# Kernel optimization log

Measured on AMD Instinct MI355X. Metric: run time of the kernel, lower is better.

## Reference

```python
import jax, jax.numpy as jnp
import numpy as np

HEAD_DIM = 64

def setup_inputs() -> dict:
    key = jax.random.key(0)
    k1, k2, k3, k4 = jax.random.split(key, 4)
    B, S, D, H = 8, 2048, 1024, HEAD_DIM
    x = jax.random.normal(k1, (B, S, D), dtype=jnp.float32)
    scale = 1.0 / np.sqrt(D)
    W_q = jax.random.normal(k2, (H, D), dtype=jnp.float32) * scale
    W_k = jax.random.normal(k3, (H, D), dtype=jnp.float32) * scale
    W_v = jax.random.normal(k4, (H, D), dtype=jnp.float32) * scale
    return {"input_embeddings": x, "W_q": W_q, "W_k": W_k, "W_v": W_v}

def reference(input_embeddings, W_q, W_k, W_v):
    # Linear(model_dim, head_dim, bias=False): y = x @ W.T
    q = jnp.einsum('bsd,hd->bsh', input_embeddings, W_q)
    k = jnp.einsum('bsd,hd->bsh', input_embeddings, W_k)
    v = jnp.einsum('bsd,hd->bsh', input_embeddings, W_v)
    scores = jnp.einsum('bqh,bkh->bqk', q, k) / jnp.sqrt(jnp.float32(HEAD_DIM))
    S = scores.shape[-1]
    causal = jnp.tril(jnp.ones((S, S), dtype=bool))  # [S,S]
    scores = jnp.where(causal, scores, -jnp.inf)
    attn = jax.nn.softmax(scores, axis=-1)
    # dropout p=0.0 (eval-equivalent): identity
    return jnp.einsum('bqk,bkh->bqh', attn, v)
```

## Files before the change

### kernel.cpp

```cpp
#include <hip/hip_runtime.h>
#include <hip/hip_bf16.h>

typedef __bf16 bf16x8 __attribute__((ext_vector_type(8)));
typedef __bf16 bf16x4 __attribute__((ext_vector_type(4)));
typedef float  f32x4  __attribute__((ext_vector_type(4)));

#define NB  8
#define SEQ 2048
#define DM  1024
#define HD  64

#define WAITV5 asm volatile("s_waitcnt vmcnt(5)" ::: "memory")
#define WAITV0 asm volatile("s_waitcnt vmcnt(0)" ::: "memory")

__device__ __forceinline__ void gll16(const void* g, void* l) {
    __builtin_amdgcn_global_load_lds(
        (const __attribute__((address_space(1))) unsigned int*)g,
        (__attribute__((address_space(3))) unsigned int*)l, 16, 0, 0);
}

__global__ void k_convw(const float* __restrict__ Wq, const float* __restrict__ Wk,
                        const float* __restrict__ Wv, __bf16* __restrict__ Wb) {
    int idx = blockIdx.x * blockDim.x + threadIdx.x;
    int e = idx * 4;
    const float* src;
    if (e < 65536)       src = Wq + e;
    else if (e < 131072) src = Wk + (e - 65536);
    else                 src = Wv + (e - 131072);
    float4 v = *reinterpret_cast<const float4*>(src);
    bf16x4 o;
    o[0] = (__bf16)v.x; o[1] = (__bf16)v.y; o[2] = (__bf16)v.z; o[3] = (__bf16)v.w;
    *reinterpret_cast<bf16x4*>(Wb + e) = o;
}

__launch_bounds__(512)
__global__ void k_proj(const float* __restrict__ X, const __bf16* __restrict__ Wb,
                       __bf16* __restrict__ Qb, __bf16* __restrict__ Kb,
                       __bf16* __restrict__ Vt) {
    __shared__ __align__(16) float  Xs[3][4096];
    __shared__ __align__(16) __bf16 Ws[3][12288];
    const int tid = threadIdx.x;
    const int w = tid >> 6, l = tid & 63;
    const int lr = l & 15, lg = l >> 4;
    const int wm = w >> 2, wn = w & 3;
    const int m0 = blockIdx.x * 64;

    const float* xsrc[2];
    #pragma unroll
    for (int j = 0; j < 2; ++j) {
        int ux = w * 128 + j * 64 + l;
        int r_ = ux >> 4, c_ = ux & 15;
        xsrc[j] = X + (size_t)(m0 + r_) * DM + (c_ ^ (r_ & 15)) * 4;
    }
    const __bf16* wsrc[3];
    #pragma unroll
    for (int j = 0; j < 3; ++j) {
        int uw = w * 192 + j * 64 + l;
        int r_ = uw >> 3, c_ = uw & 7;
        wsrc[j] = Wb + (size_t)r_ * DM + (c_ ^ (r_ & 7)) * 8;
    }

    f32x4 acc[2][3];
    #pragma unroll
    for (int mt = 0; mt < 2; ++mt)
        #pragma unroll
        for (int ct = 0; ct < 3; ++ct)
            acc[mt][ct] = f32x4{0.f, 0.f, 0.f, 0.f};

    int abase[2], bbase[3];
    #pragma unroll
    for (int mt = 0; mt < 2; ++mt) abase[mt] = (wm * 32 + mt * 16 + lr) * 64;
    #pragma unroll
    for (int ct = 0; ct < 3; ++ct) bbase[ct] = ((wn * 3 + ct) * 16 + lr) * 64;

    #pragma unroll
    for (int t = 0; t < 2; ++t) {
        #pragma unroll
        for (int j = 0; j < 2; ++j) gll16(xsrc[j] + t * 64, &Xs[t][w * 512 + j * 256]);
        #pragma unroll
        for (int j = 0; j < 3; ++j) gll16(wsrc[j] + t * 64, &Ws[t][w * 1536 + j * 512]);
    }

    int sl = 0;
    for (int t = 0; t < 16; ++t) {
        if (t < 15) WAITV5; else WAITV0;
        __builtin_amdgcn_s_barrier();
        if (t + 2 < 16) {
            int si = sl + 2; if (si >= 3) si -= 3;
            #pragma unroll
            for (int j = 0; j < 2; ++j)
                gll16(xsrc[j] + (t + 2) * 64, &Xs[si][w * 512 + j * 256]);
            #pragma unroll
            for (int j = 0; j < 3; ++j)
                gll16(wsrc[j] + (t + 2) * 64, &Ws[si][w * 1536 + j * 512]);
        }
        const float*  Xp = &Xs[sl][0];
        const __bf16* Wp = &Ws[sl][0];
        #pragma unroll
        for (int ks = 0; ks < 2; ++ks) {
            bf16x8 af[2];
            #pragma unroll
            for (int mt = 0; mt < 2; ++mt) {
                f32x4 a0 = *reinterpret_cast<const f32x4*>(Xp + abase[mt] + ((ks * 8 + lg * 2)     ^ lr) * 4);
                f32x4 a1 = *reinterpret_cast<const f32x4*>(Xp + abase[mt] + ((ks * 8 + lg * 2 + 1) ^ lr) * 4);
                #pragma unroll
                for (int j = 0; j < 4; ++j) { af[mt][j] = (__bf16)a0[j]; af[mt][4 + j] = (__bf16)a1[j]; }
            }
            #pragma unroll
            for (int ct = 0; ct < 3; ++ct) {
                bf16x8 bf = *reinterpret_cast<const bf16x8*>(
                    Wp + bbase[ct] + (((ks * 4 + lg) ^ (lr & 7)) * 8));
                #pragma unroll
                for (int mt = 0; mt < 2; ++mt)
                    acc[mt][ct] = __builtin_amdgcn_mfma_f32_16x16x32_bf16(af[mt], bf, acc[mt][ct], 0, 0, 0);
            }
        }
        ++sl; if (sl >= 3) sl = 0;
    }

    #pragma unroll
    for (int mt = 0; mt < 2; ++mt) {
        const int rowbase = m0 + wm * 32 + mt * 16 + lg * 4;
        #pragma unroll
        for (int ct = 0; ct < 3; ++ct) {
            const int ntile = wn * 3 + ct;
            const int mtx = ntile >> 2;
            const int d = (ntile & 3) * 16 + lr;
            if (mtx == 0) {
                #pragma unroll
                for (int r = 0; r < 4; ++r)
                    Qb[(size_t)(rowbase + r) * HD + d] = (__bf16)(acc[mt][ct][r] * 0.18033688f);
            } else if (mtx == 1) {
                #pragma unroll
                for (int r = 0; r < 4; ++r)
                    Kb[(size_t)(rowbase + r) * HD + d] = (__bf16)acc[mt][ct][r];
            } else {
                int bb = rowbase >> 11;
                int s0 = rowbase & 2047;
                bf16x4 vv;
                #pragma unroll
                for (int r = 0; r < 4; ++r) vv[r] = (__bf16)acc[mt][ct][r];
                *reinterpret_cast<bf16x4*>(Vt + ((size_t)bb * HD + d) * SEQ + s0) = vv;
            }
        }
    }
}

__launch_bounds__(512)
__global__ void k_attn(const __bf16* __restrict__ Qb, const __bf16* __restrict__ Kb,
                       const __bf16* __restrict__ Vt, __bf16* __restrict__ Opart,
                       float* __restrict__ ML, int T, int NC) {
    const int bid = blockIdx.x;
    const int b = bid / (16 * NC);
    const int rem = bid - b * 16 * NC;
    const int qt2 = rem / NC;
    const int c = rem - qt2 * NC;
    const int kmax = 2 * qt2 + 1;
    if (c * T > kmax) return;
    const int kt0 = c * T;
    const int nt = min(T, kmax + 1 - kt0);
    const int q0 = qt2 * 128;

    __shared__ __align__(16) __bf16 Ks[64][72];
    __shared__ __align__(16) __bf16 Vs[64][72];
    __shared__ __align__(16) __bf16 Ps[128][72];
    const int tid = threadIdx.x;
    const int w = tid >> 6, l = tid & 63;
    const int lr = l & 15, lg = l >> 4;
    const __bf16* Qp = Qb + (size_t)b * SEQ * HD;
    const __bf16* Kp = Kb + (size_t)b * SEQ * HD;
    const __bf16* Vp = Vt + (size_t)b * HD * SEQ;

    const int srow = tid >> 3, sc8 = (tid & 7) * 8;
    const int myq = q0 + 16 * w + lr;

    bf16x8 qa[2];
    #pragma unroll
    for (int ks = 0; ks < 2; ++ks)
        qa[ks] = *reinterpret_cast<const bf16x8*>(
            Qp + (size_t)myq * HD + ks * 32 + lg * 8);

    bf16x8 kpre, vpre;
    {
        const int k0 = kt0 * 64;
        kpre = *reinterpret_cast<const bf16x8*>(Kp + (size_t)(k0 + srow) * HD + sc8);
        vpre = *reinterpret_cast<const bf16x8*>(Vp + (size_t)srow * SEQ + k0 + sc8);
    }

    f32x4 oacc[4];
    #pragma unroll
    for (int r = 0; r < 4; ++r) oacc[r] = f32x4{0.f, 0.f, 0.f, 0.f};
    float m = -1e30f, lsum = 0.f;

    for (int it = 0; it < nt; ++it) {
        const int kt = kt0 + it;
        const int k0 = kt * 64;
        __syncthreads();
        *reinterpret_cast<bf16x8*>(&Ks[srow][sc8]) = kpre;
        *reinterpret_cast<bf16x8*>(&Vs[srow][sc8]) = vpre;
        __syncthreads();
        if (it + 1 < nt) {
            const int k0n = k0 + 64;
            kpre = *reinterpret_cast<const bf16x8*>(Kp + (size_t)(k0n + srow) * HD + sc8);
            vpre = *reinterpret_cast<const bf16x8*>(Vp + (size_t)srow * SEQ + k0n + sc8);
        }

        if (k0 > q0 + 16 * w + 15) continue;

        f32x4 sacc[4];
        #pragma unroll
        for (int t = 0; t < 4; ++t) sacc[t] = f32x4{0.f, 0.f, 0.f, 0.f};
        #pragma unroll
        for (int ks = 0; ks < 2; ++ks) {
            #pragma unroll
            for (int t = 0; t < 4; ++t) {
                bf16x8 kf = *reinterpret_cast<const bf16x8*>(&Ks[16 * t + lr][ks * 32 + lg * 8]);
                sacc[t] = __builtin_amdgcn_mfma_f32_16x16x32_bf16(kf, qa[ks], sacc[t], 0, 0, 0);
            }
        }

        float pmax = -1e30f;
        if (k0 + 63 > q0 + 16 * w) {
            #pragma unroll
            for (int t = 0; t < 4; ++t)
                #pragma unroll
                for (int r = 0; r < 4; ++r) {
                    float v = sacc[t][r];
                    if ((k0 + 16 * t + lg * 4 + r) > myq) v = -1e30f;
                    sacc[t][r] = v;
                    pmax = fmaxf(pmax, v);
                }
        } else {
            #pragma unroll
            for (int t = 0; t < 4; ++t)
                #pragma unroll
                for (int r = 0; r < 4; ++r) pmax = fmaxf(pmax, sacc[t][r]);
        }
        pmax = fmaxf(pmax, __shfl_xor(pmax, 16));
        pmax = fmaxf(pmax, __shfl_xor(pmax, 32));

        if (!__all(pmax <= m + 12.f)) {
            float mnew = fmaxf(m, pmax);
            float fsc = exp2f(m - mnew);
            m = mnew;
            lsum *= fsc;
            #pragma unroll
            for (int r = 0; r < 4; ++r) {
                float fq = __shfl(fsc, (l & 48) + lg * 4 + r);
                #pragma unroll
                for (int t2 = 0; t2 < 4; ++t2) oacc[t2][r] *= fq;
            }
        }

        float rs = 0.f;
        #pragma unroll
        for (int t = 0; t < 4; ++t)
            #pragma unroll
            for (int r = 0; r < 4; ++r) {
                float p = exp2f(sacc[t][r] - m);
                sacc[t][r] = p;
                rs += p;
            }
        rs += __shfl_xor(rs, 16);
        rs += __shfl_xor(rs, 32);
        lsum += rs;

        #pragma unroll
        for (int t = 0; t < 4; ++t) {
            bf16x4 pv;
            #pragma unroll
            for (int r = 0; r < 4; ++r) pv[r] = (__bf16)sacc[t][r];
            *reinterpret_cast<bf16x4*>(&Ps[16 * w + lr][16 * t + lg * 4]) = pv;
        }

        #pragma unroll
        for (int ks = 0; ks < 2; ++ks) {
            bf16x8 pa = *reinterpret_cast<const bf16x8*>(&Ps[16 * w + lr][ks * 32 + lg * 8]);
            #pragma unroll
            for (int t2 = 0; t2 < 4; ++t2) {
                bf16x8 vb = *reinterpret_cast<const bf16x8*>(&Vs[16 * t2 + lr][ks * 32 + lg * 8]);
                oacc[t2] = __builtin_amdgcn_mfma_f32_16x16x32_bf16(pa, vb, oacc[t2], 0, 0, 0);
            }
        }
    }

    const size_t slot = (size_t)bid;
    __bf16* op = Opart + slot * 8192;
    #pragma unroll
    for (int t2 = 0; t2 < 4; ++t2)
        #pragma unroll
        for (int r = 0; r < 4; ++r)
            op[(16 * w + lg * 4 + r) * 64 + 16 * t2 + lr] = (__bf16)oacc[t2][r];
    if (lg == 0) {
        float* ml = ML + slot * 256;
        int row = 16 * w + lr;
        ml[row * 2]     = m;
        ml[row * 2 + 1] = lsum;
    }
}

__launch_bounds__(512)
__global__ void k_merge(const __bf16* __restrict__ Opart, const float* __restrict__ ML,
                        float* __restrict__ Out, int T, int NC) {
    const int bq2 = blockIdx.x >> 1;
    const int half = blockIdx.x & 1;
    const int qt2 = bq2 & 15;
    const int nc = (2 * qt2 + 1) / T + 1;
    const int tid = threadIdx.x;
    const int row = tid >> 2;
    const int cg = (tid & 3) * 8 + half * 32;
    const int base = bq2 * NC;

    float M = -1e30f;
    for (int c = 0; c < nc; ++c)
        M = fmaxf(M, ML[(size_t)(base + c) * 256 + row * 2]);

    float L = 0.f;
    f32x4 a0{0,0,0,0}, a1{0,0,0,0};
    for (int c = 0; c < nc; ++c) {
        const float* ml = ML + (size_t)(base + c) * 256 + row * 2;
        float wgt = exp2f(ml[0] - M);
        L += ml[1] * wgt;
        bf16x8 v = *reinterpret_cast<const bf16x8*>(
            Opart + (size_t)(base + c) * 8192 + row * 64 + cg);
        #pragma unroll
        for (int j = 0; j < 4; ++j) {
            a0[j] += wgt * (float)v[j];
            a1[j] += wgt * (float)v[4 + j];
        }
    }
    float inv = 1.f / L;
    #pragma unroll
    for (int j = 0; j < 4; ++j) { a0[j] *= inv; a1[j] *= inv; }
    float* o = Out + ((size_t)bq2 * 128 + row) * 64 + cg;
    *reinterpret_cast<f32x4*>(o)     = a0;
    *reinterpret_cast<f32x4*>(o + 4) = a1;
}

extern "C" void kernel_launch(void* const* d_in, const int* in_sizes, int n_in,
                              void* d_out, int out_size, void* d_ws, size_t ws_size,
                              hipStream_t stream) {
    const float* x  = (const float*)d_in[0];
    const float* wq = (const float*)d_in[1];
    const float* wk = (const float*)d_in[2];
    const float* wv = (const float*)d_in[3];
    char* ws = (char*)d_ws;
    __bf16* Wb = (__bf16*)ws;
    __bf16* Qb = (__bf16*)(ws + 524288);
    __bf16* Kb = (__bf16*)(ws + 524288 + 2097152);
    __bf16* Vt = (__bf16*)(ws + 524288 + 2 * 2097152);
    const size_t base = 524288 + 3 * 2097152;
    float* out = (float*)d_out;

    int NC = (ws_size >= base + (size_t)(8 * 16 * 8) * 17408) ? 8 : 2;
    int T = 32 / NC;
    const int slots = 8 * 16 * NC;
    float*  ML    = (float*)(ws + base);
    __bf16* Opart = (__bf16*)(ws + base + (size_t)slots * 1024);

    hipLaunchKernelGGL(k_convw, dim3(192), dim3(256), 0, stream, wq, wk, wv, Wb);
    hipLaunchKernelGGL(k_proj,  dim3(256), dim3(512), 0, stream, x, Wb, Qb, Kb, Vt);
    hipLaunchKernelGGL(k_attn,  dim3(8 * 16 * NC), dim3(512), 0, stream,
                       Qb, Kb, Vt, Opart, ML, T, NC);
    hipLaunchKernelGGL(k_merge, dim3(256), dim3(512), 0, stream, Opart, ML, out, T, NC);
}
```

Before: 59.76 us.

## Restructure QKV projection: smaller row tiles, W fragments loaded straight to registers

The projection kernel now processes 32 rows per block with 4 waves, each wave owning all rows and 3 output column tiles. Weight fragments are read from global memory (L2-resident) directly into registers with double buffering, so only X goes through LDS via async loads. The grid doubles to 512 blocks. This cuts LDS footprint and traffic to raise occupancy and spread the X-read-bound projection across more CUs, at the cost of redundant per-wave W reads from L2 and more register pressure.

Result: slower. 67.11 us (+12.3%).

```diff
diff --git a/kernel.cpp b/kernel.cpp
--- a/kernel.cpp
+++ b/kernel.cpp
@@ -9,9 +9,6 @@
 #define SEQ 2048
 #define DM  1024
 #define HD  64
-
-#define WAITV5 asm volatile("s_waitcnt vmcnt(5)" ::: "memory")
-#define WAITV0 asm volatile("s_waitcnt vmcnt(0)" ::: "memory")
 
 __device__ __forceinline__ void gll16(const void* g, void* l) {
     __builtin_amdgcn_global_load_lds(
@@ -33,32 +30,62 @@
     *reinterpret_cast<bf16x4*>(Wb + e) = o;
 }
 
-__launch_bounds__(512)
+__device__ __forceinline__ void loadW(const __bf16* const (&wptr)[3], int t,
+                                      bf16x8 (&fr)[6]) {
+    #pragma unroll
+    for (int ct = 0; ct < 3; ++ct)
+        #pragma unroll
+        for (int ks = 0; ks < 2; ++ks)
+            fr[ct * 2 + ks] = *reinterpret_cast<const bf16x8*>(
+                wptr[ct] + (size_t)t * 64 + ks * 32);
+}
+
+__device__ __forceinline__ void computeT(const float* xb, int lr, int lg,
+                                         const bf16x8 (&fr)[6], f32x4 (&acc)[2][3]) {
+    #pragma unroll
+    for (int ks = 0; ks < 2; ++ks) {
+        bf16x8 af[2];
+        #pragma unroll
+        for (int mt = 0; mt < 2; ++mt) {
+            const int base = (mt * 16 + lr) * 64;
+            f32x4 a0 = *reinterpret_cast<const f32x4*>(xb + base + ((ks * 8 + lg * 2)     ^ lr) * 4);
+            f32x4 a1 = *reinterpret_cast<const f32x4*>(xb + base + ((ks * 8 + lg * 2 + 1) ^ lr) * 4);
+            #pragma unroll
+            for (int j = 0; j < 4; ++j) { af[mt][j] = (__bf16)a0[j]; af[mt][4 + j] = (__bf16)a1[j]; }
+        }
+        #pragma unroll
+        for (int ct = 0; ct < 3; ++ct)
+            #pragma unroll
+            for (int mt = 0; mt < 2; ++mt)
+                acc[mt][ct] = __builtin_amdgcn_mfma_f32_16x16x32_bf16(
+                    af[mt], fr[ct * 2 + ks], acc[mt][ct], 0, 0, 0);
+    }
+}
+
+__launch_bounds__(256)
 __global__ void k_proj(const float* __restrict__ X, const __bf16* __restrict__ Wb,
                        __bf16* __restrict__ Qb, __bf16* __restrict__ Kb,
                        __bf16* __restrict__ Vt) {
-    __shared__ __align__(16) float  Xs[3][4096];
-    __shared__ __align__(16) __bf16 Ws[3][12288];
+    __shared__ __align__(16) float Xs[3][2048];
     const int tid = threadIdx.x;
     const int w = tid >> 6, l = tid & 63;
     const int lr = l & 15, lg = l >> 4;
-    const int wm = w >> 2, wn = w & 3;
-    const int m0 = blockIdx.x * 64;
+    const int m0 = blockIdx.x * 32;
 
     const float* xsrc[2];
+    float* lb[2];
     #pragma unroll
     for (int j = 0; j < 2; ++j) {
-        int ux = w * 128 + j * 64 + l;
-        int r_ = ux >> 4, c_ = ux & 15;
+        int u = w * 64 + j * 256 + l;
+        int r_ = u >> 4, c_ = u & 15;
         xsrc[j] = X + (size_t)(m0 + r_) * DM + (c_ ^ (r_ & 15)) * 4;
-    }
-    const __bf16* wsrc[3];
-    #pragma unroll
-    for (int j = 0; j < 3; ++j) {
-        int uw = w * 192 + j * 64 + l;
-        int r_ = uw >> 3, c_ = uw & 7;
-        wsrc[j] = Wb + (size_t)r_ * DM + (c_ ^ (r_ & 7)) * 8;
-    }
+        lb[j]   = &Xs[0][0] + (w * 64 + j * 256) * 4;
+    }
+
+    const __bf16* wptr[3];
+    #pragma unroll
+    for (int ct = 0; ct < 3; ++ct)
+        wptr[ct] = Wb + (size_t)((w * 3 + ct) * 16 + lr) * DM + lg * 8;
 
     f32x4 acc[2][3];
     #pragma unroll
@@ -67,63 +94,50 @@
         for (int ct = 0; ct < 3; ++ct)
             acc[mt][ct] = f32x4{0.f, 0.f, 0.f, 0.f};
 
-    int abase[2], bbase[3];
-    #pragma unroll
-    for (int mt = 0; mt < 2; ++mt) abase[mt] = (wm * 32 + mt * 16 + lr) * 64;
-    #pragma unroll
-    for (int ct = 0; ct < 3; ++ct) bbase[ct] = ((wn * 3 + ct) * 16 + lr) * 64;
-
-    #pragma unroll
-    for (int t = 0; t < 2; ++t) {
-        #pragma unroll
-        for (int j = 0; j < 2; ++j) gll16(xsrc[j] + t * 64, &Xs[t][w * 512 + j * 256]);
-        #pragma unroll
-        for (int j = 0; j < 3; ++j) gll16(wsrc[j] + t * 64, &Ws[t][w * 1536 + j * 512]);
-    }
-
-    int sl = 0;
-    for (int t = 0; t < 16; ++t) {
-        if (t < 15) WAITV5; else WAITV0;
+    bf16x8 wA[6], wB[6];
+
+    #pragma unroll
+    for (int j = 0; j < 2; ++j) gll16(xsrc[j], lb[j]);
+    asm volatile("" ::: "memory");
+    loadW(wptr, 0, wA);
+    asm volatile("" ::: "memory");
+    #pragma unroll
+    for (int j = 0; j < 2; ++j) gll16(xsrc[j] + 64, lb[j] + 2048);
+
+    #pragma unroll
+    for (int tt = 0; tt < 7; ++tt) {
+        const int t0 = 2 * tt;
+        asm volatile("s_waitcnt vmcnt(8)" ::: "memory");
         __builtin_amdgcn_s_barrier();
-        if (t + 2 < 16) {
-            int si = sl + 2; if (si >= 3) si -= 3;
-            #pragma unroll
-            for (int j = 0; j < 2; ++j)
-                gll16(xsrc[j] + (t + 2) * 64, &Xs[si][w * 512 + j * 256]);
-            #pragma unroll
-            for (int j = 0; j < 3; ++j)
-                gll16(wsrc[j] + (t + 2) * 64, &Ws[si][w * 1536 + j * 512]);
-        }
-        const float*  Xp = &Xs[sl][0];
-        const __bf16* Wp = &Ws[sl][0];
-        #pragma unroll
-        for (int ks = 0; ks < 2; ++ks) {
-            bf16x8 af[2];
-            #pragma unroll
-            for (int mt = 0; mt < 2; ++mt) {
-                f32x4 a0 = *reinterpret_cast<const f32x4*>(Xp + abase[mt] + ((ks * 8 + lg * 2)     ^ lr) * 4);
-                f32x4 a1 = *reinterpret_cast<const f32x4*>(Xp + abase[mt] + ((ks * 8 + lg * 2 + 1) ^ lr) * 4);
-                #pragma unroll
-                for (int j = 0; j < 4; ++j) { af[mt][j] = (__bf16)a0[j]; af[mt][4 + j] = (__bf16)a1[j]; }
-            }
-            #pragma unroll
-            for (int ct = 0; ct < 3; ++ct) {
-                bf16x8 bf = *reinterpret_cast<const bf16x8*>(
-                    Wp + bbase[ct] + (((ks * 4 + lg) ^ (lr & 7)) * 8));
-                #pragma unroll
-                for (int mt = 0; mt < 2; ++mt)
-                    acc[mt][ct] = __builtin_amdgcn_mfma_f32_16x16x32_bf16(af[mt], bf, acc[mt][ct], 0, 0, 0);
-            }
-        }
-        ++sl; if (sl >= 3) sl = 0;
-    }
+        loadW(wptr, t0 + 1, wB);
+        asm volatile("" ::: "memory");
+        #pragma unroll
+        for (int j = 0; j < 2; ++j)
+            gll16(xsrc[j] + (size_t)(t0 + 2) * 64, lb[j] + ((t0 + 2) % 3) * 2048);
+        computeT(&Xs[t0 % 3][0], lr, lg, wA, acc);
+        asm volatile("s_waitcnt vmcnt(8)" ::: "memory");
+        __builtin_amdgcn_s_barrier();
+        loadW(wptr, t0 + 2, wA);
+        asm volatile("" ::: "memory");
+        #pragma unroll
+        for (int j = 0; j < 2; ++j)
+            gll16(xsrc[j] + (size_t)(t0 + 3) * 64, lb[j] + ((t0 + 3) % 3) * 2048);
+        computeT(&Xs[(t0 + 1) % 3][0], lr, lg, wB, acc);
+    }
+    asm volatile("s_waitcnt vmcnt(8)" ::: "memory");
+    __builtin_amdgcn_s_barrier();
+    loadW(wptr, 15, wB);
+    computeT(&Xs[14 % 3][0], lr, lg, wA, acc);
+    asm volatile("s_waitcnt vmcnt(0)" ::: "memory");
+    __builtin_amdgcn_s_barrier();
+    computeT(&Xs[15 % 3][0], lr, lg, wB, acc);
 
     #pragma unroll
     for (int mt = 0; mt < 2; ++mt) {
-        const int rowbase = m0 + wm * 32 + mt * 16 + lg * 4;
+        const int rowbase = m0 + mt * 16 + lg * 4;
         #pragma unroll
         for (int ct = 0; ct < 3; ++ct) {
-            const int ntile = wn * 3 + ct;
+            const int ntile = w * 3 + ct;
             const int mtx = ntile >> 2;
             const int d = (ntile & 3) * 16 + lr;
             if (mtx == 0) {
@@ -359,7 +373,7 @@
     __bf16* Opart = (__bf16*)(ws + base + (size_t)slots * 1024);
 
     hipLaunchKernelGGL(k_convw, dim3(192), dim3(256), 0, stream, wq, wk, wv, Wb);
-    hipLaunchKernelGGL(k_proj,  dim3(256), dim3(512), 0, stream, x, Wb, Qb, Kb, Vt);
+    hipLaunchKernelGGL(k_proj,  dim3(512), dim3(256), 0, stream, x, Wb, Qb, Kb, Vt);
     hipLaunchKernelGGL(k_attn,  dim3(8 * 16 * NC), dim3(512), 0, stream,
                        Qb, Kb, Vt, Opart, ML, T, NC);
     hipLaunchKernelGGL(k_merge, dim3(256), dim3(512), 0, stream, Opart, ML, out, T, NC);
```

## Switch projection to double-buffered LDS pipeline and reduce attention split count

Applied to the files above, without the earlier changes.

The projection kernel's three-stage LDS ring is reduced to a two-buffer ping-pong with one tile of prefetch, which lowers LDS use. The kernel also gains a launch-bounds occupancy hint and a fully unrolled main loop. Separately, the attention key-split count drops from 8 to 4 chunks per query block, halving the partial outputs the merge kernel must combine but giving the attention kernel fewer blocks. The shallower prefetch may expose more global-load latency per tile.

After: 55.02 us. -7.9%, faster.

```diff
diff --git a/kernel.cpp b/kernel.cpp
--- a/kernel.cpp
+++ b/kernel.cpp
@@ -33,12 +33,12 @@
     *reinterpret_cast<bf16x4*>(Wb + e) = o;
 }
 
-__launch_bounds__(512)
+__launch_bounds__(512, 4)
 __global__ void k_proj(const float* __restrict__ X, const __bf16* __restrict__ Wb,
                        __bf16* __restrict__ Qb, __bf16* __restrict__ Kb,
                        __bf16* __restrict__ Vt) {
-    __shared__ __align__(16) float  Xs[3][4096];
-    __shared__ __align__(16) __bf16 Ws[3][12288];
+    __shared__ __align__(16) float  Xs[2][4096];
+    __shared__ __align__(16) __bf16 Ws[2][12288];
     const int tid = threadIdx.x;
     const int w = tid >> 6, l = tid & 63;
     const int lr = l & 15, lg = l >> 4;
@@ -48,15 +48,15 @@
     const float* xsrc[2];
     #pragma unroll
     for (int j = 0; j < 2; ++j) {
-        int ux = w * 128 + j * 64 + l;
-        int r_ = ux >> 4, c_ = ux & 15;
+        int u = w * 128 + j * 64 + l;
+        int r_ = u >> 4, c_ = u & 15;
         xsrc[j] = X + (size_t)(m0 + r_) * DM + (c_ ^ (r_ & 15)) * 4;
     }
     const __bf16* wsrc[3];
     #pragma unroll
     for (int j = 0; j < 3; ++j) {
-        int uw = w * 192 + j * 64 + l;
-        int r_ = uw >> 3, c_ = uw & 7;
+        int u = w * 192 + j * 64 + l;
+        int r_ = u >> 3, c_ = u & 7;
         wsrc[j] = Wb + (size_t)r_ * DM + (c_ ^ (r_ & 7)) * 8;
     }
 
@@ -74,28 +74,27 @@
     for (int ct = 0; ct < 3; ++ct) bbase[ct] = ((wn * 3 + ct) * 16 + lr) * 64;
 
     #pragma unroll
-    for (int t = 0; t < 2; ++t) {
-        #pragma unroll
-        for (int j = 0; j < 2; ++j) gll16(xsrc[j] + t * 64, &Xs[t][w * 512 + j * 256]);
-        #pragma unroll
-        for (int j = 0; j < 3; ++j) gll16(wsrc[j] + t * 64, &Ws[t][w * 1536 + j * 512]);
-    }
-
-    int sl = 0;
+    for (int j = 0; j < 2; ++j) gll16(xsrc[j], &Xs[0][w * 512 + j * 256]);
+    #pragma unroll
+    for (int j = 0; j < 3; ++j) gll16(wsrc[j], &Ws[0][w * 1536 + j * 512]);
+
+    #pragma unroll
     for (int t = 0; t < 16; ++t) {
-        if (t < 15) WAITV5; else WAITV0;
+        const int cur = t & 1;
         __builtin_amdgcn_s_barrier();
-        if (t + 2 < 16) {
-            int si = sl + 2; if (si >= 3) si -= 3;
+        if (t + 1 < 16) {
             #pragma unroll
             for (int j = 0; j < 2; ++j)
-                gll16(xsrc[j] + (t + 2) * 64, &Xs[si][w * 512 + j * 256]);
+                gll16(xsrc[j] + (size_t)(t + 1) * 64, &Xs[cur ^ 1][w * 512 + j * 256]);
             #pragma unroll
             for (int j = 0; j < 3; ++j)
-                gll16(wsrc[j] + (t + 2) * 64, &Ws[si][w * 1536 + j * 512]);
-        }
-        const float*  Xp = &Xs[sl][0];
-        const __bf16* Wp = &Ws[sl][0];
+                gll16(wsrc[j] + (size_t)(t + 1) * 64, &Ws[cur ^ 1][w * 1536 + j * 512]);
+            WAITV5;
+        } else {
+            WAITV0;
+        }
+        const float*  Xp = &Xs[cur][0];
+        const __bf16* Wp = &Ws[cur][0];
         #pragma unroll
         for (int ks = 0; ks < 2; ++ks) {
             bf16x8 af[2];
@@ -112,10 +111,10 @@
                     Wp + bbase[ct] + (((ks * 4 + lg) ^ (lr & 7)) * 8));
                 #pragma unroll
                 for (int mt = 0; mt < 2; ++mt)
-                    acc[mt][ct] = __builtin_amdgcn_mfma_f32_16x16x32_bf16(af[mt], bf, acc[mt][ct], 0, 0, 0);
-            }
-        }
-        ++sl; if (sl >= 3) sl = 0;
+                    acc[mt][ct] = __builtin_amdgcn_mfma_f32_16x16x32_bf16(
+                        af[mt], bf, acc[mt][ct], 0, 0, 0);
+            }
+        }
     }
 
     #pragma unroll
@@ -352,7 +351,7 @@
     const size_t base = 524288 + 3 * 2097152;
     float* out = (float*)d_out;
 
-    int NC = (ws_size >= base + (size_t)(8 * 16 * 8) * 17408) ? 8 : 2;
+    int NC = (ws_size >= base + (size_t)(8 * 16 * 4) * 17408) ? 4 : 2;
     int T = 32 / NC;
     const int slots = 8 * 16 * NC;
     float*  ML    = (float*)(ws + base);
```
